# Kernel tuning notes

Hardware: AMD Instinct MI355X
Metric: run time of the kernel (lower is better)

Reference implementation:

```python
import jax, jax.numpy as jnp
import numpy as np

N_HEAD = 16
BLOCK_SIZE = 2049  # w2 last dim = block_size - 1 = 2048


def setup_inputs() -> dict:
    key = jax.random.key(0)
    ks = jax.random.split(key, 9)
    B, T, C = 2, 2048, 1024
    hd = C // N_HEAD
    M = BLOCK_SIZE - 1
    return {
        "x": jax.random.normal(ks[0], (B, T, C), jnp.float32),
        "w1_w": jax.random.normal(ks[1], (C, C), jnp.float32) * 0.02,
        "w1_b": jax.random.normal(ks[2], (C,), jnp.float32) * 0.02,
        # torch uniform_(a=-0.001, b=0.001)
        "w2": jax.random.uniform(ks[3], (N_HEAD, hd, M), jnp.float32, -0.001, 0.001),
        "b2": jax.random.normal(ks[4], (M,), jnp.float32) * 0.02,
        "value_w": jax.random.normal(ks[5], (C, C), jnp.float32) * 0.02,
        "value_b": jax.random.normal(ks[6], (C,), jnp.float32) * 0.02,
        "proj_w": jax.random.normal(ks[7], (C, C), jnp.float32) * 0.02,
        "proj_b": jax.random.normal(ks[8], (C,), jnp.float32) * 0.02,
    }


def reference(x, w1_w, w1_b, w2, b2, value_w, value_b, proj_w, proj_b):
    B, T, C = x.shape
    H = N_HEAD
    hd = C // H
    M = w2.shape[-1]  # block_size - 1
    # kernel = relu(w1(x)), split heads -> [B, H, T, hd]
    k = jax.nn.relu(x @ w1_w.T + w1_b).reshape(B, T, H, hd).transpose(0, 2, 1, 3)
    # synthesizer scores: [B, H, T, M]
    attn = jnp.einsum('bhtd,hdm->bhtm', k, w2) + b2
    # causal mask = tril(ones(block,block))[:T, :M] == 0 -> -inf
    causal = jnp.tril(jnp.ones((T, M), dtype=bool))
    attn = jnp.where(causal, attn, -jnp.inf)
    # softmax over first T score columns
    attn = jax.nn.softmax(attn[..., :T], axis=-1)  # [B, H, T, T]
    v = (x @ value_w.T + value_b).reshape(B, T, H, hd).transpose(0, 2, 1, 3)
    out = jnp.einsum('bhts,bhsd->bhtd', attn, v)
    out = out.transpose(0, 2, 1, 3).reshape(B, T, C)
    return out @ proj_w.T + proj_b
```

## Files before the change

kernel.cpp:

```cpp
#include <hip/hip_runtime.h>
#include <math.h>
#include <stdint.h>

typedef __bf16 bf16;
typedef __bf16 bf16x8 __attribute__((ext_vector_type(8)));
typedef __bf16 bf16x4 __attribute__((ext_vector_type(4)));
typedef float f32x4 __attribute__((ext_vector_type(4)));
typedef unsigned int u32;

__device__ __forceinline__ int swz(int row, int chunk) {
    return row * 64 + ((chunk ^ (row & 7)) << 3);
}

__device__ __forceinline__ void gld16(void* lds, const void* g) {
    __builtin_amdgcn_global_load_lds(
        (const __attribute__((address_space(1))) u32*)g,
        (__attribute__((address_space(3))) u32*)lds, 16, 0, 0);
}

__device__ __forceinline__ void stage64(bf16* dst, const bf16* src, size_t srcStride,
                                        int w, int l) {
    #pragma unroll
    for (int i = 0; i < 2; ++i) {
        const int br = (w * 2 + i) * 8;
        const int r = br + (l >> 3);
        const int gs = (l & 7) ^ (r & 7);
        gld16(dst + br * 64, src + (size_t)r * srcStride + gs * 8);
    }
}

__global__ void cast_bf16_k(const float* __restrict__ src, bf16* __restrict__ dst, int n) {
    const int stride = gridDim.x * blockDim.x * 4;
    for (int i = (blockIdx.x * blockDim.x + threadIdx.x) * 4; i < n; i += stride) {
        float4 v = *(const float4*)(src + i);
        bf16x4 o = {(bf16)v.x, (bf16)v.y, (bf16)v.z, (bf16)v.w};
        *(bf16x4*)(dst + i) = o;
    }
}

__global__ __launch_bounds__(256) void w2_transpose_k(const float* __restrict__ w2,
                                                      bf16* __restrict__ w2t, int M) {
    __shared__ float Tf[64][65];
    const int h = blockIdx.y, m0 = blockIdx.x * 64, t = threadIdx.x;
    {
        const int dr = t >> 4, c4 = (t & 15) * 4;
        #pragma unroll
        for (int it = 0; it < 4; ++it) {
            const int d = dr + it * 16;
            float4 v = *(const float4*)(w2 + ((size_t)h * 64 + d) * M + m0 + c4);
            Tf[d][c4] = v.x; Tf[d][c4 + 1] = v.y; Tf[d][c4 + 2] = v.z; Tf[d][c4 + 3] = v.w;
        }
    }
    __syncthreads();
    const int m = t >> 2;
    #pragma unroll
    for (int it = 0; it < 2; ++it) {
        const int ch = (t & 3) + it * 4;
        bf16x8 o;
        #pragma unroll
        for (int j = 0; j < 8; ++j) o[j] = (bf16)Tf[ch * 8 + j][m];
        *(bf16x8*)(w2t + ((size_t)h * M + m0 + m) * 64 + ch * 8) = o;
    }
}

__global__ __launch_bounds__(256) void gemm_bf16_k(const bf16* __restrict__ A,
                                                   const bf16* __restrict__ Bw,
                                                   const float* __restrict__ bias,
                                                   const float* __restrict__ bias2,
                                                   float* __restrict__ C0,
                                                   bf16* __restrict__ CK,
                                                   bf16* __restrict__ CV,
                                                   int M, int N, int K, int mode, int Ns)
{
    __shared__ __align__(16) bf16 As[128 * 64];
    __shared__ __align__(16) bf16 Bs[128 * 64];
    const int tid = threadIdx.x;
    const int w = tid >> 6, l = tid & 63;
    const int wr = w >> 1, wc = w & 1;
    const int lc = l & 15, lg = l >> 4;
    const int row0 = blockIdx.y * 128, col0 = blockIdx.x * 128;

    f32x4 acc[4][4] = {};

    for (int k0 = 0; k0 < K; k0 += 64) {
        __syncthreads();
        #pragma unroll
        for (int i = 0; i < 4; ++i) {
            const int br = (w * 4 + i) * 8;
            const int r = br + (l >> 3);
            const int gs = (l & 7) ^ (r & 7);
            gld16(As + br * 64, A  + (size_t)(row0 + r) * K + k0 + gs * 8);
            gld16(Bs + br * 64, Bw + (size_t)(col0 + r) * K + k0 + gs * 8);
        }
        __syncthreads();
        #pragma unroll
        for (int ks = 0; ks < 2; ++ks) {
            bf16x8 af[4], bfv[4];
            #pragma unroll
            for (int i = 0; i < 4; ++i) {
                af[i]  = *(const bf16x8*)&As[swz(wr * 64 + i * 16 + lc, ks * 4 + lg)];
                bfv[i] = *(const bf16x8*)&Bs[swz(wc * 64 + i * 16 + lc, ks * 4 + lg)];
            }
            #pragma unroll
            for (int mi = 0; mi < 4; ++mi)
                #pragma unroll
                for (int ni = 0; ni < 4; ++ni)
                    acc[mi][ni] = __builtin_amdgcn_mfma_f32_16x16x32_bf16(af[mi], bfv[ni], acc[mi][ni], 0, 0, 0);
        }
    }

    #pragma unroll
    for (int ni = 0; ni < 4; ++ni) {
        const int col = col0 + wc * 64 + ni * 16 + lc;
        #pragma unroll
        for (int mi = 0; mi < 4; ++mi) {
            const int rowb = row0 + wr * 64 + mi * 16 + lg * 4;
            f32x4 v = acc[mi][ni];
            if (mode == 0) {
                const float bv = bias[col];
                #pragma unroll
                for (int r = 0; r < 4; ++r)
                    C0[(size_t)(rowb + r) * N + col] = v[r] + bv;
            } else if (col < Ns) {
                const float bv = bias[col];
                #pragma unroll
                for (int r = 0; r < 4; ++r)
                    CK[(size_t)(rowb + r) * Ns + col] = (bf16)fmaxf(v[r] + bv, 0.f);
            } else {
                const float bv = bias2[col - Ns];
                const int b = rowb >> 11, tt = rowb & 2047;
                bf16x4 o = {(bf16)(v[0] + bv), (bf16)(v[1] + bv),
                            (bf16)(v[2] + bv), (bf16)(v[3] + bv)};
                *(bf16x4*)(CV + ((size_t)b * Ns + (col - Ns)) * 2048 + tt) = o;
            }
        }
    }
}

__device__ __forceinline__ void tile_step(bf16x8 kf0, bf16x8 kf1,
                                          const bf16* Wb, const bf16* Vb,
                                          bf16* Pw, const float (&bb)[4],
                                          f32x4 (&acc)[4], float (&lsum)[4],
                                          bool diag, int lc, int lg, int w)
{
    f32x4 sv[4];
    #pragma unroll
    for (int st = 0; st < 4; ++st) sv[st] = {bb[st], bb[st], bb[st], bb[st]};
    #pragma unroll
    for (int st = 0; st < 4; ++st) {
        bf16x8 wb0 = *(const bf16x8*)&Wb[swz(st * 16 + lc, lg)];
        bf16x8 wb1 = *(const bf16x8*)&Wb[swz(st * 16 + lc, 4 + lg)];
        sv[st] = __builtin_amdgcn_mfma_f32_16x16x32_bf16(kf0, wb0, sv[st], 0, 0, 0);
        sv[st] = __builtin_amdgcn_mfma_f32_16x16x32_bf16(kf1, wb1, sv[st], 0, 0, 0);
    }
    #pragma unroll
    for (int st = 0; st < 4; ++st) {
        const int scol = st * 16 + lc;
        #pragma unroll
        for (int r = 0; r < 4; ++r) {
            float e = __expf(sv[st][r]);
            if (diag && scol > w * 16 + lg * 4 + r) e = 0.f;
            lsum[r] += e;
            const int trow = lg * 4 + r;
            Pw[trow * 64 + (((scol >> 3) ^ (trow & 7)) << 3) + (scol & 7)] = (bf16)e;
        }
    }
    #pragma unroll
    for (int ks = 0; ks < 2; ++ks) {
        bf16x8 pf = *(const bf16x8*)&Pw[swz(lc, ks * 4 + lg)];
        #pragma unroll
        for (int dt = 0; dt < 4; ++dt) {
            bf16x8 vv = *(const bf16x8*)&Vb[swz(dt * 16 + lc, ks * 4 + lg)];
            acc[dt] = __builtin_amdgcn_mfma_f32_16x16x32_bf16(pf, vv, acc[dt], 0, 0, 0);
        }
    }
}

__global__ __launch_bounds__(256, 2) void synth_attn_v7(const bf16* __restrict__ Kb,
                                                        const bf16* __restrict__ VT,
                                                        const bf16* __restrict__ w2t,
                                                        const float* __restrict__ b2,
                                                        bf16* __restrict__ Ob)
{
    constexpr int T = 2048, C = 1024, M = 2048;
    __shared__ __align__(16) bf16 Wl[3][64 * 64];
    __shared__ __align__(16) bf16 Vl[3][64 * 64];
    __shared__ __align__(16) bf16 Pl[4][16 * 64];
    const int tid = threadIdx.x;
    const int w = tid >> 6, l = tid & 63;
    const int lc = l & 15, lg = l >> 4;

    const int bx = blockIdx.x;
    const int half = bx >> 8, idx = bx & 255;
    const int jj = idx & 15;
    const int j = half ? (15 - jj) : jj;
    const int bh = (half << 4) | (idx >> 4);
    const int h = bh & 15, b = bh >> 4;
    const int tA = j, tB = 31 - j;
    const int t0A = tA * 64, t0B = tB * 64;

    const bf16* Wgt = w2t + (size_t)h * M * 64;
    const bf16* Vgt = VT + ((size_t)b * C + h * 64) * T;
    bf16* Pw = &Pl[w][0];

    const bf16* KgA = Kb + (size_t)(b * T + t0A + w * 16 + lc) * C + h * 64;
    const bf16* KgB = Kb + (size_t)(b * T + t0B + w * 16 + lc) * C + h * 64;
    const bf16x8 kfA0 = *(const bf16x8*)(KgA + lg * 8);
    const bf16x8 kfA1 = *(const bf16x8*)(KgA + 32 + lg * 8);
    const bf16x8 kfB0 = *(const bf16x8*)(KgB + lg * 8);
    const bf16x8 kfB1 = *(const bf16x8*)(KgB + 32 + lg * 8);

    f32x4 accA[4] = {}, accB[4] = {};
    float lsA[4] = {0.f, 0.f, 0.f, 0.f}, lsB[4] = {0.f, 0.f, 0.f, 0.f};

    stage64(&Wl[0][0], Wgt, 64, w, l);
    stage64(&Vl[0][0], Vgt, T, w, l);
    stage64(&Wl[1][0], Wgt + (size_t)64 * 64, 64, w, l);
    stage64(&Vl[1][0], Vgt + 64, T, w, l);

    int cur = 0;
    for (int sb = 0; sb <= tB; ++sb) {
        const int s0 = sb * 64;
        if (sb < tB) asm volatile("s_waitcnt vmcnt(4)" ::: "memory");
        else         asm volatile("s_waitcnt vmcnt(0)" ::: "memory");
        __builtin_amdgcn_s_barrier();

        float bb[4];
        #pragma unroll
        for (int st = 0; st < 4; ++st) bb[st] = b2[s0 + st * 16 + lc];

        tile_step(kfB0, kfB1, &Wl[cur][0], &Vl[cur][0], Pw, bb, accB, lsB,
                  sb == tB, lc, lg, w);
        if (sb <= tA)
            tile_step(kfA0, kfA1, &Wl[cur][0], &Vl[cur][0], Pw, bb, accA, lsA,
                      sb == tA, lc, lg, w);

        if (sb + 2 <= tB) {
            int nx = cur + 2; if (nx >= 3) nx -= 3;
            stage64(&Wl[nx][0], Wgt + (size_t)(s0 + 128) * 64, 64, w, l);
            stage64(&Vl[nx][0], Vgt + (s0 + 128), T, w, l);
        }
        if (++cur == 3) cur = 0;
    }

    #pragma unroll
    for (int r = 0; r < 4; ++r) {
        float la = lsA[r], lb = lsB[r];
        la += __shfl_xor(la, 1); la += __shfl_xor(la, 2);
        la += __shfl_xor(la, 4); la += __shfl_xor(la, 8);
        lb += __shfl_xor(lb, 1); lb += __shfl_xor(lb, 2);
        lb += __shfl_xor(lb, 4); lb += __shfl_xor(lb, 8);
        const float ia = 1.f / la, ib = 1.f / lb;
        bf16* dA = Ob + (size_t)(b * T + t0A + w * 16 + lg * 4 + r) * C + h * 64;
        bf16* dB = Ob + (size_t)(b * T + t0B + w * 16 + lg * 4 + r) * C + h * 64;
        #pragma unroll
        for (int dt = 0; dt < 4; ++dt) {
            dA[dt * 16 + lc] = (bf16)(accA[dt][r] * ia);
            dB[dt * 16 + lc] = (bf16)(accB[dt][r] * ib);
        }
    }
}

extern "C" void kernel_launch(void* const* d_in, const int* in_sizes, int n_in,
                              void* d_out, int out_size, void* d_ws, size_t ws_size,
                              hipStream_t stream) {
    const float* x       = (const float*)d_in[0];
    const float* w1_w    = (const float*)d_in[1];
    const float* w1_b    = (const float*)d_in[2];
    const float* w2      = (const float*)d_in[3];
    const float* b2      = (const float*)d_in[4];
    const float* value_w = (const float*)d_in[5];
    const float* value_b = (const float*)d_in[6];
    const float* proj_w  = (const float*)d_in[7];
    const float* proj_b  = (const float*)d_in[8];

    const int B = 2, T = 2048, C = 1024, H = 16, M = 2048;
    const int R = B * T;

    bf16* xb  = (bf16*)d_ws;
    bf16* w1b = xb  + (size_t)R * C;
    bf16* vwb = w1b + (size_t)C * C;
    bf16* w2t = vwb + (size_t)C * C;
    bf16* pwb = w2t + (size_t)H * M * 64;
    bf16* Kb  = pwb + (size_t)C * C;
    bf16* VTb = Kb  + (size_t)R * C;
    bf16* Ob  = VTb + (size_t)R * C;

    cast_bf16_k<<<1024, 256, 0, stream>>>(x, xb, R * C);
    cast_bf16_k<<<256, 256, 0, stream>>>(w1_w, w1b, C * C);
    cast_bf16_k<<<256, 256, 0, stream>>>(value_w, vwb, C * C);
    cast_bf16_k<<<256, 256, 0, stream>>>(proj_w, pwb, C * C);
    w2_transpose_k<<<dim3(M / 64, H), 256, 0, stream>>>(w2, w2t, M);

    gemm_bf16_k<<<dim3(2 * C / 128, R / 128), 256, 0, stream>>>(
        xb, w1b, w1_b, value_b, nullptr, Kb, VTb, R, 2 * C, C, 1, C);

    synth_attn_v7<<<dim3(512), 256, 0, stream>>>(Kb, VTb, w2t, b2, Ob);

    gemm_bf16_k<<<dim3(C / 128, R / 128), 256, 0, stream>>>(
        Ob, pwb, proj_b, nullptr, (float*)d_out, nullptr, nullptr, R, C, C, 0, C);
}
```

Measured before the change: 116.1 us.

## Split paired query tiles across 8 waves and fuse weight cast kernels

The attention kernel now uses 512 threads per block. Waves 0-3 handle the late query tile and waves 4-7 the early one, so each wave owns a single tile instead of processing both serially. The shared W/V tiles are staged with one 16-byte load per thread, and b2 is preloaded into LDS. Block-to-tile mapping is simplified by dropping the half-swapped ordering. Three weight cast launches are merged into one kernel. The upper-half waves go idle once their tile's causal range ends, and LDS use grows by 8KB for b2 plus extra P buffers.

```diff
diff --git a/kernel.cpp b/kernel.cpp
--- a/kernel.cpp
+++ b/kernel.cpp
@@ -18,15 +18,12 @@
         (__attribute__((address_space(3))) u32*)lds, 16, 0, 0);
 }
 
-__device__ __forceinline__ void stage64(bf16* dst, const bf16* src, size_t srcStride,
-                                        int w, int l) {
-    #pragma unroll
-    for (int i = 0; i < 2; ++i) {
-        const int br = (w * 2 + i) * 8;
-        const int r = br + (l >> 3);
-        const int gs = (l & 7) ^ (r & 7);
-        gld16(dst + br * 64, src + (size_t)r * srcStride + gs * 8);
-    }
+__device__ __forceinline__ void stage8(bf16* dst, const bf16* src, size_t srcStride,
+                                       int w, int l) {
+    const int br = w * 8;
+    const int r = br + (l >> 3);
+    const int gs = (l & 7) ^ (r & 7);
+    gld16(dst + br * 64, src + (size_t)r * srcStride + gs * 8);
 }
 
 __global__ void cast_bf16_k(const float* __restrict__ src, bf16* __restrict__ dst, int n) {
@@ -35,6 +32,23 @@
         float4 v = *(const float4*)(src + i);
         bf16x4 o = {(bf16)v.x, (bf16)v.y, (bf16)v.z, (bf16)v.w};
         *(bf16x4*)(dst + i) = o;
+    }
+}
+
+__global__ void cast3_bf16_k(const float* __restrict__ s0, bf16* __restrict__ d0,
+                             const float* __restrict__ s1, bf16* __restrict__ d1,
+                             const float* __restrict__ s2, bf16* __restrict__ d2, int n) {
+    const int stride = gridDim.x * blockDim.x * 4;
+    for (int i = (blockIdx.x * blockDim.x + threadIdx.x) * 4; i < n; i += stride) {
+        float4 v0 = *(const float4*)(s0 + i);
+        float4 v1 = *(const float4*)(s1 + i);
+        float4 v2 = *(const float4*)(s2 + i);
+        bf16x4 o0 = {(bf16)v0.x, (bf16)v0.y, (bf16)v0.z, (bf16)v0.w};
+        bf16x4 o1 = {(bf16)v1.x, (bf16)v1.y, (bf16)v1.z, (bf16)v1.w};
+        bf16x4 o2 = {(bf16)v2.x, (bf16)v2.y, (bf16)v2.z, (bf16)v2.w};
+        *(bf16x4*)(d0 + i) = o0;
+        *(bf16x4*)(d1 + i) = o1;
+        *(bf16x4*)(d2 + i) = o2;
     }
 }
 
@@ -139,10 +153,13 @@
 
 __device__ __forceinline__ void tile_step(bf16x8 kf0, bf16x8 kf1,
                                           const bf16* Wb, const bf16* Vb,
-                                          bf16* Pw, const float (&bb)[4],
+                                          bf16* Pw, const float* b2l, int s0,
                                           f32x4 (&acc)[4], float (&lsum)[4],
-                                          bool diag, int lc, int lg, int w)
+                                          bool diag, int lc, int lg, int wq)
 {
+    float bb[4];
+    #pragma unroll
+    for (int st = 0; st < 4; ++st) bb[st] = b2l[s0 + st * 16 + lc];
     f32x4 sv[4];
     #pragma unroll
     for (int st = 0; st < 4; ++st) sv[st] = {bb[st], bb[st], bb[st], bb[st]};
@@ -159,7 +176,7 @@
         #pragma unroll
         for (int r = 0; r < 4; ++r) {
             float e = __expf(sv[st][r]);
-            if (diag && scol > w * 16 + lg * 4 + r) e = 0.f;
+            if (diag && scol > wq * 16 + lg * 4 + r) e = 0.f;
             lsum[r] += e;
             const int trow = lg * 4 + r;
             Pw[trow * 64 + (((scol >> 3) ^ (trow & 7)) << 3) + (scol & 7)] = (bf16)e;
@@ -176,7 +193,7 @@
     }
 }
 
-__global__ __launch_bounds__(256, 2) void synth_attn_v7(const bf16* __restrict__ Kb,
+__global__ __launch_bounds__(512, 4) void synth_attn_v8(const bf16* __restrict__ Kb,
                                                         const bf16* __restrict__ VT,
                                                         const bf16* __restrict__ w2t,
                                                         const float* __restrict__ b2,
@@ -185,79 +202,69 @@
     constexpr int T = 2048, C = 1024, M = 2048;
     __shared__ __align__(16) bf16 Wl[3][64 * 64];
     __shared__ __align__(16) bf16 Vl[3][64 * 64];
-    __shared__ __align__(16) bf16 Pl[4][16 * 64];
+    __shared__ __align__(16) bf16 Pl[8][16 * 64];
+    __shared__ float b2l[M];
     const int tid = threadIdx.x;
     const int w = tid >> 6, l = tid & 63;
     const int lc = l & 15, lg = l >> 4;
+    const int wq = w & 3, wt = w >> 2;
 
     const int bx = blockIdx.x;
-    const int half = bx >> 8, idx = bx & 255;
-    const int jj = idx & 15;
-    const int j = half ? (15 - jj) : jj;
-    const int bh = (half << 4) | (idx >> 4);
+    const int j = bx & 15;
+    const int bh = bx >> 4;
     const int h = bh & 15, b = bh >> 4;
     const int tA = j, tB = 31 - j;
-    const int t0A = tA * 64, t0B = tB * 64;
+    const int myT = wt ? tA : tB;
+    const int t0 = myT * 64;
+
+    *(float4*)&b2l[tid * 4] = *(const float4*)(b2 + tid * 4);
+    __syncthreads();
 
     const bf16* Wgt = w2t + (size_t)h * M * 64;
     const bf16* Vgt = VT + ((size_t)b * C + h * 64) * T;
     bf16* Pw = &Pl[w][0];
 
-    const bf16* KgA = Kb + (size_t)(b * T + t0A + w * 16 + lc) * C + h * 64;
-    const bf16* KgB = Kb + (size_t)(b * T + t0B + w * 16 + lc) * C + h * 64;
-    const bf16x8 kfA0 = *(const bf16x8*)(KgA + lg * 8);
-    const bf16x8 kfA1 = *(const bf16x8*)(KgA + 32 + lg * 8);
-    const bf16x8 kfB0 = *(const bf16x8*)(KgB + lg * 8);
-    const bf16x8 kfB1 = *(const bf16x8*)(KgB + 32 + lg * 8);
-
-    f32x4 accA[4] = {}, accB[4] = {};
-    float lsA[4] = {0.f, 0.f, 0.f, 0.f}, lsB[4] = {0.f, 0.f, 0.f, 0.f};
-
-    stage64(&Wl[0][0], Wgt, 64, w, l);
-    stage64(&Vl[0][0], Vgt, T, w, l);
-    stage64(&Wl[1][0], Wgt + (size_t)64 * 64, 64, w, l);
-    stage64(&Vl[1][0], Vgt + 64, T, w, l);
+    const bf16* Kg = Kb + (size_t)(b * T + t0 + wq * 16 + lc) * C + h * 64;
+    const bf16x8 kf0 = *(const bf16x8*)(Kg + lg * 8);
+    const bf16x8 kf1 = *(const bf16x8*)(Kg + 32 + lg * 8);
+
+    stage8(&Wl[0][0], Wgt, 64, w, l);
+    stage8(&Vl[0][0], Vgt, T, w, l);
+    stage8(&Wl[1][0], Wgt + (size_t)64 * 64, 64, w, l);
+    stage8(&Vl[1][0], Vgt + 64, T, w, l);
+
+    f32x4 acc[4] = {};
+    float lsum[4] = {0.f, 0.f, 0.f, 0.f};
 
     int cur = 0;
     for (int sb = 0; sb <= tB; ++sb) {
         const int s0 = sb * 64;
-        if (sb < tB) asm volatile("s_waitcnt vmcnt(4)" ::: "memory");
+        if (sb < tB) asm volatile("s_waitcnt vmcnt(2)" ::: "memory");
         else         asm volatile("s_waitcnt vmcnt(0)" ::: "memory");
         __builtin_amdgcn_s_barrier();
 
-        float bb[4];
-        #pragma unroll
-        for (int st = 0; st < 4; ++st) bb[st] = b2[s0 + st * 16 + lc];
-
-        tile_step(kfB0, kfB1, &Wl[cur][0], &Vl[cur][0], Pw, bb, accB, lsB,
-                  sb == tB, lc, lg, w);
-        if (sb <= tA)
-            tile_step(kfA0, kfA1, &Wl[cur][0], &Vl[cur][0], Pw, bb, accA, lsA,
-                      sb == tA, lc, lg, w);
+        if (sb <= myT)
+            tile_step(kf0, kf1, &Wl[cur][0], &Vl[cur][0], Pw, b2l, s0,
+                      acc, lsum, sb == myT, lc, lg, wq);
 
         if (sb + 2 <= tB) {
             int nx = cur + 2; if (nx >= 3) nx -= 3;
-            stage64(&Wl[nx][0], Wgt + (size_t)(s0 + 128) * 64, 64, w, l);
-            stage64(&Vl[nx][0], Vgt + (s0 + 128), T, w, l);
+            stage8(&Wl[nx][0], Wgt + (size_t)(s0 + 128) * 64, 64, w, l);
+            stage8(&Vl[nx][0], Vgt + (s0 + 128), T, w, l);
         }
         if (++cur == 3) cur = 0;
     }
 
     #pragma unroll
     for (int r = 0; r < 4; ++r) {
-        float la = lsA[r], lb = lsB[r];
-        la += __shfl_xor(la, 1); la += __shfl_xor(la, 2);
-        la += __shfl_xor(la, 4); la += __shfl_xor(la, 8);
-        lb += __shfl_xor(lb, 1); lb += __shfl_xor(lb, 2);
-        lb += __shfl_xor(lb, 4); lb += __shfl_xor(lb, 8);
-        const float ia = 1.f / la, ib = 1.f / lb;
-        bf16* dA = Ob + (size_t)(b * T + t0A + w * 16 + lg * 4 + r) * C + h * 64;
-        bf16* dB = Ob + (size_t)(b * T + t0B + w * 16 + lg * 4 + r) * C + h * 64;
-        #pragma unroll
-        for (int dt = 0; dt < 4; ++dt) {
-            dA[dt * 16 + lc] = (bf16)(accA[dt][r] * ia);
-            dB[dt * 16 + lc] = (bf16)(accB[dt][r] * ib);
-        }
+        float ls = lsum[r];
+        ls += __shfl_xor(ls, 1); ls += __shfl_xor(ls, 2);
+        ls += __shfl_xor(ls, 4); ls += __shfl_xor(ls, 8);
+        const float inv = 1.f / ls;
+        bf16* dst = Ob + (size_t)(b * T + t0 + wq * 16 + lg * 4 + r) * C + h * 64;
+        #pragma unroll
+        for (int dt = 0; dt < 4; ++dt)
+            dst[dt * 16 + lc] = (bf16)(acc[dt][r] * inv);
     }
 }
 
@@ -287,15 +294,13 @@
     bf16* Ob  = VTb + (size_t)R * C;
 
     cast_bf16_k<<<1024, 256, 0, stream>>>(x, xb, R * C);
-    cast_bf16_k<<<256, 256, 0, stream>>>(w1_w, w1b, C * C);
-    cast_bf16_k<<<256, 256, 0, stream>>>(value_w, vwb, C * C);
-    cast_bf16_k<<<256, 256, 0, stream>>>(proj_w, pwb, C * C);
+    cast3_bf16_k<<<512, 256, 0, stream>>>(w1_w, w1b, value_w, vwb, proj_w, pwb, C * C);
     w2_transpose_k<<<dim3(M / 64, H), 256, 0, stream>>>(w2, w2t, M);
 
     gemm_bf16_k<<<dim3(2 * C / 128, R / 128), 256, 0, stream>>>(
         xb, w1b, w1_b, value_b, nullptr, Kb, VTb, R, 2 * C, C, 1, C);
 
-    synth_attn_v7<<<dim3(512), 256, 0, stream>>>(Kb, VTb, w2t, b2, Ob);
+    synth_attn_v8<<<dim3(512), 512, 0, stream>>>(Kb, VTb, w2t, b2, Ob);
 
     gemm_bf16_k<<<dim3(C / 128, R / 128), 256, 0, stream>>>(
         Ob, pwb, proj_b, nullptr, (float*)d_out, nullptr, nullptr, R, C, C, 0, C);
```

Measured after the change: 111.5 us. 3.9% less time.
